# Optimization experiments

Hardware: AMD Instinct MI355X
Metric: run time of the kernel (lower is better)

The kernel has to match this reference:

```python
import jax, jax.numpy as jnp
import numpy as np

MARGIN = 9.0  # args.transe_margin
B, N, D = 32, 200000, 64


def setup_inputs() -> dict:
    key = jax.random.key(0)
    k1, k2, k3 = jax.random.split(key, 3)
    s_emb = jax.random.normal(k1, (B, D), dtype=jnp.float32)
    rel_emb = jax.random.normal(k2, (B, D), dtype=jnp.float32)
    emb_e = jax.random.normal(k3, (N, D), dtype=jnp.float32)
    return {"s_emb": s_emb, "rel_emb": rel_emb, "emb_e": emb_e}


def reference(s_emb, rel_emb, emb_e):
    # mode='rhs': pred = margin - || (s + r)[b,None,:] - emb_e[None,:,:] ||_2 over D
    # dropout with p=0.0 is identity.
    query = s_emb + rel_emb                      # (B, D)
    diff = query[:, None, :] - emb_e[None, :, :]  # (B, N, D) broadcast intermediate
    # stable L2 norm over last dim
    pred = MARGIN - jnp.sqrt(jnp.sum(diff * diff, axis=-1))  # (B, N)
    return pred
```

## Files before the change

kernel.cpp:

```cpp
#include <hip/hip_runtime.h>


#define MARGIN 9.0f

typedef __attribute__((ext_vector_type(8)))  short bf16x8;
typedef __attribute__((ext_vector_type(16))) float f32x16;
typedef __attribute__((ext_vector_type(4)))  unsigned int u32x4;

typedef __attribute__((address_space(3))) void        lds_vp;
typedef __attribute__((address_space(1))) const void  glb_vp;

__device__ __forceinline__ unsigned eswz(unsigned p) {
    return p ^ (((p >> 8) & 15u) << 4);
}

__global__ __launch_bounds__(128, 3)
void transe12(const float* __restrict__ s_emb,
              const float* __restrict__ rel_emb,
              const float* __restrict__ emb_e,
              float* __restrict__ out, int N)
{
    __shared__ __align__(16) char lds[32768];
    const int t = threadIdx.x, w = t >> 6, lane = t & 63;
    const int m = lane & 31, h = lane >> 5;
    char* const b0 = lds + w * 16384;
    char* const b1 = b0 + 8192;
    const int  nt32 = N >> 5;
    const long T0   = (long)blockIdx.x * 8 + w * 4;

    const float4* s4 = (const float4*)s_emb;
    const float4* r4 = (const float4*)rel_emb;
    float4 sv[8], rv[8];
#pragma unroll
    for (int k = 0; k < 8; ++k) sv[k] = s4[k*64 + lane];
#pragma unroll
    for (int k = 0; k < 8; ++k) rv[k] = r4[k*64 + lane];

    auto dma8 = [&](long tile, char* l) {
        const long ts = (tile < nt32) ? tile : (long)(nt32 - 1);
        const char* g = (const char*)emb_e + ts * 8192;
#pragma unroll
        for (int k = 0; k < 8; ++k) {
            const unsigned p = (unsigned)(k*1024 + lane*16);
            __builtin_amdgcn_global_load_lds((glb_vp*)(g + eswz(p)),
                                             (lds_vp*)(l + k*1024), 16, 0, 0);
        }
    };

    dma8(T0 + 1, b1);

#pragma unroll
    for (int k = 0; k < 8; ++k) {
        const unsigned p = (unsigned)(k*1024 + lane*16);
        float4 q = make_float4(sv[k].x+rv[k].x, sv[k].y+rv[k].y,
                               sv[k].z+rv[k].z, sv[k].w+rv[k].w);
        *(float4*)(b0 + eswz(p)) = q;
    }
    asm volatile("s_waitcnt lgkmcnt(0)" ::: "memory");

    const unsigned fb = (unsigned)(m*256 + h*32);
    bf16x8 qh[4], ql[4];
    float qn_part = 0.f;
#pragma unroll
    for (int tt = 0; tt < 4; ++tt) {
        const unsigned pe = eswz(fb + tt*64);
        float4 q0 = *(const float4*)(b0 + pe);
        float4 q1 = *(const float4*)(b0 + (pe ^ 16));
        const float qf[8] = {q0.x,q0.y,q0.z,q0.w, q1.x,q1.y,q1.z,q1.w};
#pragma unroll
        for (int i = 0; i < 8; ++i) {
            const float f = qf[i];
            qn_part = fmaf(f, f, qn_part);
            const unsigned u = __float_as_uint(f);
            qh[tt][i] = (short)(u >> 16);
            const float lo = f - __uint_as_float(u & 0xFFFF0000u);
            ql[tt][i] = (short)(__float_as_uint(lo) >> 16);
        }
    }
    const float qn_own = qn_part + __shfl_xor(qn_part, 32);
    float qn_all[32];
#pragma unroll
    for (int i = 0; i < 32; ++i)
        qn_all[i] = __uint_as_float(
            __builtin_amdgcn_readlane(__float_as_uint(qn_own), i));

    asm volatile("s_waitcnt lgkmcnt(0)" ::: "memory");
    dma8(T0 + 0, b0);

    auto compute_tile = [&](const char* L, f32x16& acc) {
#pragma unroll
        for (int i = 0; i < 16; ++i) acc[i] = 0.f;
        float en_part = 0.f;
#pragma unroll
        for (int tt = 0; tt < 4; ++tt) {
            const unsigned pe = eswz(fb + tt*64);
            float4 e0 = *(const float4*)(L + pe);
            float4 e1 = *(const float4*)(L + (pe ^ 16));
            en_part = fmaf(e0.x, e0.x, en_part);
            en_part = fmaf(e0.y, e0.y, en_part);
            en_part = fmaf(e0.z, e0.z, en_part);
            en_part = fmaf(e0.w, e0.w, en_part);
            en_part = fmaf(e1.x, e1.x, en_part);
            en_part = fmaf(e1.y, e1.y, en_part);
            en_part = fmaf(e1.z, e1.z, en_part);
            en_part = fmaf(e1.w, e1.w, en_part);
            u32x4 ep;
            ep[0] = __builtin_amdgcn_perm(__float_as_uint(e0.y),
                                          __float_as_uint(e0.x), 0x07060302u);
            ep[1] = __builtin_amdgcn_perm(__float_as_uint(e0.w),
                                          __float_as_uint(e0.z), 0x07060302u);
            ep[2] = __builtin_amdgcn_perm(__float_as_uint(e1.y),
                                          __float_as_uint(e1.x), 0x07060302u);
            ep[3] = __builtin_amdgcn_perm(__float_as_uint(e1.w),
                                          __float_as_uint(e1.z), 0x07060302u);
            const bf16x8 eh = __builtin_bit_cast(bf16x8, ep);
            acc = __builtin_amdgcn_mfma_f32_32x32x16_bf16(qh[tt], eh, acc, 0,0,0);
            acc = __builtin_amdgcn_mfma_f32_32x32x16_bf16(ql[tt], eh, acc, 0,0,0);
        }
        const float en = en_part + __shfl_xor(en_part, 32);
#pragma unroll
        for (int r = 0; r < 16; ++r) {
            const int bb = (r & 3) + 8*(r >> 2);
            const float qn_v = h ? qn_all[bb + 4] : qn_all[bb];
            const float d2 = fmaxf(fmaf(-2.f, acc[r], qn_v + en), 0.f);
            acc[r] = MARGIN - sqrtf(d2);
        }
    };

    f32x16 p0, p1, p2, p3;
    asm volatile("s_waitcnt vmcnt(8)" ::: "memory");
    compute_tile(b1, p1);
    asm volatile("s_waitcnt lgkmcnt(0)" ::: "memory");
    dma8(T0 + 2, b1);
    asm volatile("s_waitcnt vmcnt(8)" ::: "memory");
    compute_tile(b0, p0);
    asm volatile("s_waitcnt lgkmcnt(0)" ::: "memory");
    dma8(T0 + 3, b0);
    asm volatile("s_waitcnt vmcnt(8)" ::: "memory");
    compute_tile(b1, p2);
    asm volatile("s_waitcnt vmcnt(0)" ::: "memory");
    compute_tile(b0, p3);

    __syncthreads();
    float* oT = (float*)lds;
    const int nlb = w*128 + m;
#pragma unroll
    for (int r = 0; r < 16; ++r) {
        const int b = (r & 3) + 8*(r >> 2) + 4*h;
        oT[b*256 + nlb +  0] = p0[r];
        oT[b*256 + nlb + 32] = p1[r];
        oT[b*256 + nlb + 64] = p2[r];
        oT[b*256 + nlb + 96] = p3[r];
    }
    __syncthreads();

    const long nb = (long)blockIdx.x * 256;
#pragma unroll
    for (int k = 0; k < 16; ++k) {
        const int  rb  = w*16 + k;
        const long col = nb + lane*4;
        if (col + 3 < N) {
            const float4 v = *(const float4*)(oT + rb*256 + lane*4);
            *(float4*)(out + (size_t)rb * N + col) = v;
        }
    }
}

extern "C" void kernel_launch(void* const* d_in, const int* in_sizes, int n_in,
                              void* d_out, int out_size, void* d_ws, size_t ws_size,
                              hipStream_t stream) {
    const float* s = (const float*)d_in[0];
    const float* r = (const float*)d_in[1];
    const float* e = (const float*)d_in[2];
    float* out = (float*)d_out;

    const int N = in_sizes[2] / 64;
    const int grid = (N + 255) / 256;

    transe12<<<grid, 128, 0, stream>>>(s, r, e, out, N);
}
```

Measured before the change: 20.23 us.

## Switch to 16x16x32 MFMA with 4 waves per 256-column block

Replaces the 32x32x16 bf16 MFMA tiling with 16x16x32 MFMAs computing two 16-row halves of the batch per wave. Blocks grow from 2 to 4 waves, each streaming four 16-entity tiles through smaller double buffers. Query norms are gathered with shuffles instead of 32 readlanes, which cuts register pressure. The goal is more waves in flight to hide memory latency, at the cost of more MFMA instructions and more LDS traffic per entity.

```diff
diff --git a/kernel.cpp b/kernel.cpp
--- a/kernel.cpp
+++ b/kernel.cpp
@@ -3,9 +3,8 @@
 
 #define MARGIN 9.0f
 
-typedef __attribute__((ext_vector_type(8)))  short bf16x8;
-typedef __attribute__((ext_vector_type(16))) float f32x16;
-typedef __attribute__((ext_vector_type(4)))  unsigned int u32x4;
+typedef __attribute__((ext_vector_type(8))) short bf16x8;
+typedef __attribute__((ext_vector_type(4))) float f32x4;
 
 typedef __attribute__((address_space(3))) void        lds_vp;
 typedef __attribute__((address_space(1))) const void  glb_vp;
@@ -14,19 +13,20 @@
     return p ^ (((p >> 8) & 15u) << 4);
 }
 
-__global__ __launch_bounds__(128, 3)
-void transe12(const float* __restrict__ s_emb,
+__global__ __launch_bounds__(256, 4)
+void transe13(const float* __restrict__ s_emb,
               const float* __restrict__ rel_emb,
               const float* __restrict__ emb_e,
               float* __restrict__ out, int N)
 {
     __shared__ __align__(16) char lds[32768];
     const int t = threadIdx.x, w = t >> 6, lane = t & 63;
-    const int m = lane & 31, h = lane >> 5;
-    char* const b0 = lds + w * 16384;
-    char* const b1 = b0 + 8192;
-    const int  nt32 = N >> 5;
-    const long T0   = (long)blockIdx.x * 8 + w * 4;
+    const int c16 = lane & 15;
+    const int g   = lane >> 4;
+    char* const B0 = lds + w * 8192;
+    char* const B1 = B0 + 4096;
+    const int  ntile = N >> 4;
+    const long Tw = (long)blockIdx.x * 16 + w * 4;
 
     const float4* s4 = (const float4*)s_emb;
     const float4* r4 = (const float4*)rel_emb;
@@ -36,128 +36,136 @@
 #pragma unroll
     for (int k = 0; k < 8; ++k) rv[k] = r4[k*64 + lane];
 
-    auto dma8 = [&](long tile, char* l) {
-        const long ts = (tile < nt32) ? tile : (long)(nt32 - 1);
-        const char* g = (const char*)emb_e + ts * 8192;
+    auto dma4 = [&](long tile, char* l) {
+        const long ts = (tile < ntile) ? tile : (long)(ntile - 1);
+        const char* gp = (const char*)emb_e + ts * 4096;
 #pragma unroll
-        for (int k = 0; k < 8; ++k) {
+        for (int k = 0; k < 4; ++k) {
             const unsigned p = (unsigned)(k*1024 + lane*16);
-            __builtin_amdgcn_global_load_lds((glb_vp*)(g + eswz(p)),
+            __builtin_amdgcn_global_load_lds((glb_vp*)(gp + eswz(p)),
                                              (lds_vp*)(l + k*1024), 16, 0, 0);
         }
     };
+    dma4(Tw + 0, B1);
 
-    dma8(T0 + 1, b1);
+    const unsigned fbase = (unsigned)(c16*256 + g*32);
+    bf16x8 qh[2][2], ql[2][2];
+    float qnp[2];
+#pragma unroll
+    for (int mh = 0; mh < 2; ++mh) {
+#pragma unroll
+        for (int k = 0; k < 4; ++k) {
+            const int kk = mh*4 + k;
+            const unsigned p = (unsigned)(k*1024 + lane*16);
+            float4 q = make_float4(sv[kk].x+rv[kk].x, sv[kk].y+rv[kk].y,
+                                   sv[kk].z+rv[kk].z, sv[kk].w+rv[kk].w);
+            *(float4*)(B0 + eswz(p)) = q;
+        }
+        asm volatile("s_waitcnt lgkmcnt(0)" ::: "memory");
+        float qq = 0.f;
+#pragma unroll
+        for (int ks = 0; ks < 2; ++ks) {
+            const unsigned pe = eswz(fbase + ks*128);
+            float4 q0 = *(const float4*)(B0 + pe);
+            float4 q1 = *(const float4*)(B0 + (pe ^ 16));
+            const float qf[8] = {q0.x,q0.y,q0.z,q0.w, q1.x,q1.y,q1.z,q1.w};
+#pragma unroll
+            for (int i = 0; i < 8; ++i) {
+                const float f = qf[i];
+                qq = fmaf(f, f, qq);
+                const unsigned u = __float_as_uint(f);
+                qh[mh][ks][i] = (short)(u >> 16);
+                const float lo = f - __uint_as_float(u & 0xFFFF0000u);
+                ql[mh][ks][i] = (short)(__float_as_uint(lo) >> 16);
+            }
+        }
+        qnp[mh] = qq;
+        asm volatile("s_waitcnt lgkmcnt(0)" ::: "memory");
+    }
+    dma4(Tw + 1, B0);
 
+    float qn0 = qnp[0]; qn0 += __shfl_xor(qn0, 16); qn0 += __shfl_xor(qn0, 32);
+    float qn1 = qnp[1]; qn1 += __shfl_xor(qn1, 16); qn1 += __shfl_xor(qn1, 32);
+    float qn_need[8];
 #pragma unroll
-    for (int k = 0; k < 8; ++k) {
-        const unsigned p = (unsigned)(k*1024 + lane*16);
-        float4 q = make_float4(sv[k].x+rv[k].x, sv[k].y+rv[k].y,
-                               sv[k].z+rv[k].z, sv[k].w+rv[k].w);
-        *(float4*)(b0 + eswz(p)) = q;
+    for (int j = 0; j < 4; ++j) {
+        qn_need[j]     = __shfl(qn0, g*4 + j);
+        qn_need[4 + j] = __shfl(qn1, g*4 + j);
     }
-    asm volatile("s_waitcnt lgkmcnt(0)" ::: "memory");
 
-    const unsigned fb = (unsigned)(m*256 + h*32);
-    bf16x8 qh[4], ql[4];
-    float qn_part = 0.f;
+    auto tile_full = [&](const char* L, f32x4& o0, f32x4& o1) {
+        f32x4 a0 = {0.f,0.f,0.f,0.f}, a1 = {0.f,0.f,0.f,0.f};
+        float ep = 0.f;
 #pragma unroll
-    for (int tt = 0; tt < 4; ++tt) {
-        const unsigned pe = eswz(fb + tt*64);
-        float4 q0 = *(const float4*)(b0 + pe);
-        float4 q1 = *(const float4*)(b0 + (pe ^ 16));
-        const float qf[8] = {q0.x,q0.y,q0.z,q0.w, q1.x,q1.y,q1.z,q1.w};
-#pragma unroll
-        for (int i = 0; i < 8; ++i) {
-            const float f = qf[i];
-            qn_part = fmaf(f, f, qn_part);
-            const unsigned u = __float_as_uint(f);
-            qh[tt][i] = (short)(u >> 16);
-            const float lo = f - __uint_as_float(u & 0xFFFF0000u);
-            ql[tt][i] = (short)(__float_as_uint(lo) >> 16);
-        }
-    }
-    const float qn_own = qn_part + __shfl_xor(qn_part, 32);
-    float qn_all[32];
-#pragma unroll
-    for (int i = 0; i < 32; ++i)
-        qn_all[i] = __uint_as_float(
-            __builtin_amdgcn_readlane(__float_as_uint(qn_own), i));
-
-    asm volatile("s_waitcnt lgkmcnt(0)" ::: "memory");
-    dma8(T0 + 0, b0);
-
-    auto compute_tile = [&](const char* L, f32x16& acc) {
-#pragma unroll
-        for (int i = 0; i < 16; ++i) acc[i] = 0.f;
-        float en_part = 0.f;
-#pragma unroll
-        for (int tt = 0; tt < 4; ++tt) {
-            const unsigned pe = eswz(fb + tt*64);
+        for (int ks = 0; ks < 2; ++ks) {
+            const unsigned pe = eswz(fbase + ks*128);
             float4 e0 = *(const float4*)(L + pe);
             float4 e1 = *(const float4*)(L + (pe ^ 16));
-            en_part = fmaf(e0.x, e0.x, en_part);
-            en_part = fmaf(e0.y, e0.y, en_part);
-            en_part = fmaf(e0.z, e0.z, en_part);
-            en_part = fmaf(e0.w, e0.w, en_part);
-            en_part = fmaf(e1.x, e1.x, en_part);
-            en_part = fmaf(e1.y, e1.y, en_part);
-            en_part = fmaf(e1.z, e1.z, en_part);
-            en_part = fmaf(e1.w, e1.w, en_part);
-            u32x4 ep;
-            ep[0] = __builtin_amdgcn_perm(__float_as_uint(e0.y),
+            ep = fmaf(e0.x, e0.x, ep); ep = fmaf(e0.y, e0.y, ep);
+            ep = fmaf(e0.z, e0.z, ep); ep = fmaf(e0.w, e0.w, ep);
+            ep = fmaf(e1.x, e1.x, ep); ep = fmaf(e1.y, e1.y, ep);
+            ep = fmaf(e1.z, e1.z, ep); ep = fmaf(e1.w, e1.w, ep);
+            unsigned ew[4];
+            ew[0] = __builtin_amdgcn_perm(__float_as_uint(e0.y),
                                           __float_as_uint(e0.x), 0x07060302u);
-            ep[1] = __builtin_amdgcn_perm(__float_as_uint(e0.w),
+            ew[1] = __builtin_amdgcn_perm(__float_as_uint(e0.w),
                                           __float_as_uint(e0.z), 0x07060302u);
-            ep[2] = __builtin_amdgcn_perm(__float_as_uint(e1.y),
+            ew[2] = __builtin_amdgcn_perm(__float_as_uint(e1.y),
                                           __float_as_uint(e1.x), 0x07060302u);
-            ep[3] = __builtin_amdgcn_perm(__float_as_uint(e1.w),
+            ew[3] = __builtin_amdgcn_perm(__float_as_uint(e1.w),
                                           __float_as_uint(e1.z), 0x07060302u);
-            const bf16x8 eh = __builtin_bit_cast(bf16x8, ep);
-            acc = __builtin_amdgcn_mfma_f32_32x32x16_bf16(qh[tt], eh, acc, 0,0,0);
-            acc = __builtin_amdgcn_mfma_f32_32x32x16_bf16(ql[tt], eh, acc, 0,0,0);
+            bf16x8 eh;
+            __builtin_memcpy(&eh, ew, 16);
+            a0 = __builtin_amdgcn_mfma_f32_16x16x32_bf16(qh[0][ks], eh, a0, 0,0,0);
+            a0 = __builtin_amdgcn_mfma_f32_16x16x32_bf16(ql[0][ks], eh, a0, 0,0,0);
+            a1 = __builtin_amdgcn_mfma_f32_16x16x32_bf16(qh[1][ks], eh, a1, 0,0,0);
+            a1 = __builtin_amdgcn_mfma_f32_16x16x32_bf16(ql[1][ks], eh, a1, 0,0,0);
         }
-        const float en = en_part + __shfl_xor(en_part, 32);
+        float en = ep; en += __shfl_xor(en, 16); en += __shfl_xor(en, 32);
 #pragma unroll
-        for (int r = 0; r < 16; ++r) {
-            const int bb = (r & 3) + 8*(r >> 2);
-            const float qn_v = h ? qn_all[bb + 4] : qn_all[bb];
-            const float d2 = fmaxf(fmaf(-2.f, acc[r], qn_v + en), 0.f);
-            acc[r] = MARGIN - sqrtf(d2);
+        for (int j = 0; j < 4; ++j) {
+            const float d0 = fmaxf(fmaf(-2.f, a0[j], qn_need[j]     + en), 0.f);
+            const float d1 = fmaxf(fmaf(-2.f, a1[j], qn_need[4 + j] + en), 0.f);
+            o0[j] = MARGIN - sqrtf(d0);
+            o1[j] = MARGIN - sqrtf(d1);
         }
     };
 
-    f32x16 p0, p1, p2, p3;
-    asm volatile("s_waitcnt vmcnt(8)" ::: "memory");
-    compute_tile(b1, p1);
+    f32x4 p00, p01, p10, p11, p20, p21, p30, p31;
+    asm volatile("s_waitcnt vmcnt(4)" ::: "memory");
+    tile_full(B1, p00, p01);
     asm volatile("s_waitcnt lgkmcnt(0)" ::: "memory");
-    dma8(T0 + 2, b1);
-    asm volatile("s_waitcnt vmcnt(8)" ::: "memory");
-    compute_tile(b0, p0);
+    dma4(Tw + 2, B1);
+    asm volatile("s_waitcnt vmcnt(4)" ::: "memory");
+    tile_full(B0, p10, p11);
     asm volatile("s_waitcnt lgkmcnt(0)" ::: "memory");
-    dma8(T0 + 3, b0);
-    asm volatile("s_waitcnt vmcnt(8)" ::: "memory");
-    compute_tile(b1, p2);
+    dma4(Tw + 3, B0);
+    asm volatile("s_waitcnt vmcnt(4)" ::: "memory");
+    tile_full(B1, p20, p21);
     asm volatile("s_waitcnt vmcnt(0)" ::: "memory");
-    compute_tile(b0, p3);
+    tile_full(B0, p30, p31);
 
     __syncthreads();
     float* oT = (float*)lds;
-    const int nlb = w*128 + m;
+    const int nl = w*64 + c16;
 #pragma unroll
-    for (int r = 0; r < 16; ++r) {
-        const int b = (r & 3) + 8*(r >> 2) + 4*h;
-        oT[b*256 + nlb +  0] = p0[r];
-        oT[b*256 + nlb + 32] = p1[r];
-        oT[b*256 + nlb + 64] = p2[r];
-        oT[b*256 + nlb + 96] = p3[r];
+    for (int j = 0; j < 4; ++j) {
+        const int b0r = g*4 + j, b1r = 16 + g*4 + j;
+        oT[b0r*256 + nl +  0] = p00[j];
+        oT[b1r*256 + nl +  0] = p01[j];
+        oT[b0r*256 + nl + 16] = p10[j];
+        oT[b1r*256 + nl + 16] = p11[j];
+        oT[b0r*256 + nl + 32] = p20[j];
+        oT[b1r*256 + nl + 32] = p21[j];
+        oT[b0r*256 + nl + 48] = p30[j];
+        oT[b1r*256 + nl + 48] = p31[j];
     }
     __syncthreads();
 
     const long nb = (long)blockIdx.x * 256;
 #pragma unroll
-    for (int k = 0; k < 16; ++k) {
-        const int  rb  = w*16 + k;
+    for (int k = 0; k < 8; ++k) {
+        const int  rb  = w*8 + k;
         const long col = nb + lane*4;
         if (col + 3 < N) {
             const float4 v = *(const float4*)(oT + rb*256 + lane*4);
@@ -177,5 +185,5 @@
     const int N = in_sizes[2] / 64;
     const int grid = (N + 255) / 256;
 
-    transe12<<<grid, 128, 0, stream>>>(s, r, e, out, N);
+    transe13<<<grid, 256, 0, stream>>>(s, r, e, out, N);
 }
```

After: 20.66 us. 2.1% more time.

## Load entity tiles into registers and stage to LDS instead of direct DMA

Applied to the files above, without the earlier changes.

Replaces the direct global-to-LDS DMA of emb_e tiles with register loads through inline asm, written into LDS just before each tile is computed. s_emb and rel_emb now go straight to LDS by DMA, and their sum is formed when the query fragments are read. Occupancy hint drops from 3 to 2 waves per EU, and scheduling barriers are added. The goal is to issue all tile loads up front with simpler waits, at the cost of more registers and extra LDS write traffic per tile.

```diff
diff --git a/kernel.cpp b/kernel.cpp
--- a/kernel.cpp
+++ b/kernel.cpp
@@ -14,8 +14,12 @@
     return p ^ (((p >> 8) & 15u) << 4);
 }
 
-__global__ __launch_bounds__(128, 3)
-void transe12(const float* __restrict__ s_emb,
+#define VMWAIT(n) do { \
+    asm volatile("s_waitcnt vmcnt(" #n ")" ::: "memory"); \
+    __builtin_amdgcn_sched_barrier(0); } while (0)
+
+__global__ __launch_bounds__(128, 2)
+void transe17(const float* __restrict__ s_emb,
               const float* __restrict__ rel_emb,
               const float* __restrict__ emb_e,
               float* __restrict__ out, int N)
@@ -28,17 +32,7 @@
     const int  nt32 = N >> 5;
     const long T0   = (long)blockIdx.x * 8 + w * 4;
 
-    const float4* s4 = (const float4*)s_emb;
-    const float4* r4 = (const float4*)rel_emb;
-    float4 sv[8], rv[8];
-#pragma unroll
-    for (int k = 0; k < 8; ++k) sv[k] = s4[k*64 + lane];
-#pragma unroll
-    for (int k = 0; k < 8; ++k) rv[k] = r4[k*64 + lane];
-
-    auto dma8 = [&](long tile, char* l) {
-        const long ts = (tile < nt32) ? tile : (long)(nt32 - 1);
-        const char* g = (const char*)emb_e + ts * 8192;
+    auto dma8g = [&](const char* g, char* l) {
 #pragma unroll
         for (int k = 0; k < 8; ++k) {
             const unsigned p = (unsigned)(k*1024 + lane*16);
@@ -46,27 +40,36 @@
                                              (lds_vp*)(l + k*1024), 16, 0, 0);
         }
     };
+    dma8g((const char*)s_emb,   b0);
+    dma8g((const char*)rel_emb, b1);
+    __builtin_amdgcn_sched_barrier(0);
 
-    dma8(T0 + 1, b1);
+    float4 E0[8], E1[8];
+    auto eload = [&](long tile, float4 (&E)[8]) {
+        const long ts = (tile < nt32) ? tile : (long)(nt32 - 1);
+        const char* g = (const char*)emb_e + ts * 8192 + (unsigned)(lane * 16);
+#pragma unroll
+        for (int k = 0; k < 8; ++k) {
+            asm volatile("global_load_dwordx4 %0, %1, off"
+                         : "=&v"(E[k]) : "v"(g + k*1024) : "memory");
+        }
+    };
+    eload(T0 + 0, E0);
+    eload(T0 + 1, E1);
 
-#pragma unroll
-    for (int k = 0; k < 8; ++k) {
-        const unsigned p = (unsigned)(k*1024 + lane*16);
-        float4 q = make_float4(sv[k].x+rv[k].x, sv[k].y+rv[k].y,
-                               sv[k].z+rv[k].z, sv[k].w+rv[k].w);
-        *(float4*)(b0 + eswz(p)) = q;
-    }
-    asm volatile("s_waitcnt lgkmcnt(0)" ::: "memory");
-
+    VMWAIT(16);
     const unsigned fb = (unsigned)(m*256 + h*32);
     bf16x8 qh[4], ql[4];
     float qn_part = 0.f;
 #pragma unroll
     for (int tt = 0; tt < 4; ++tt) {
         const unsigned pe = eswz(fb + tt*64);
-        float4 q0 = *(const float4*)(b0 + pe);
-        float4 q1 = *(const float4*)(b0 + (pe ^ 16));
-        const float qf[8] = {q0.x,q0.y,q0.z,q0.w, q1.x,q1.y,q1.z,q1.w};
+        float4 s0 = *(const float4*)(b0 + pe);
+        float4 s1 = *(const float4*)(b0 + (pe ^ 16));
+        float4 r0 = *(const float4*)(b1 + pe);
+        float4 r1 = *(const float4*)(b1 + (pe ^ 16));
+        const float qf[8] = { s0.x+r0.x, s0.y+r0.y, s0.z+r0.z, s0.w+r0.w,
+                              s1.x+r1.x, s1.y+r1.y, s1.z+r1.z, s1.w+r1.w };
 #pragma unroll
         for (int i = 0; i < 8; ++i) {
             const float f = qf[i];
@@ -83,9 +86,16 @@
     for (int i = 0; i < 32; ++i)
         qn_all[i] = __uint_as_float(
             __builtin_amdgcn_readlane(__float_as_uint(qn_own), i));
+    asm volatile("s_waitcnt lgkmcnt(0)" ::: "memory");
+    __builtin_amdgcn_sched_barrier(0);
 
-    asm volatile("s_waitcnt lgkmcnt(0)" ::: "memory");
-    dma8(T0 + 0, b0);
+    auto stage = [&](const float4 (&E)[8], char* l) {
+#pragma unroll
+        for (int k = 0; k < 8; ++k) {
+            const unsigned p = (unsigned)(k*1024 + lane*16);
+            *(float4*)(l + eswz(p)) = E[k];
+        }
+    };
 
     auto compute_tile = [&](const char* L, f32x16& acc) {
 #pragma unroll
@@ -128,18 +138,20 @@
     };
 
     f32x16 p0, p1, p2, p3;
-    asm volatile("s_waitcnt vmcnt(8)" ::: "memory");
+    VMWAIT(8);
+    stage(E0, b0);
+    eload(T0 + 2, E0);
+    compute_tile(b0, p0);
+    VMWAIT(8);
+    stage(E1, b1);
+    eload(T0 + 3, E1);
     compute_tile(b1, p1);
-    asm volatile("s_waitcnt lgkmcnt(0)" ::: "memory");
-    dma8(T0 + 2, b1);
-    asm volatile("s_waitcnt vmcnt(8)" ::: "memory");
-    compute_tile(b0, p0);
-    asm volatile("s_waitcnt lgkmcnt(0)" ::: "memory");
-    dma8(T0 + 3, b0);
-    asm volatile("s_waitcnt vmcnt(8)" ::: "memory");
-    compute_tile(b1, p2);
-    asm volatile("s_waitcnt vmcnt(0)" ::: "memory");
-    compute_tile(b0, p3);
+    VMWAIT(8);
+    stage(E0, b0);
+    compute_tile(b0, p2);
+    VMWAIT(0);
+    stage(E1, b1);
+    compute_tile(b1, p3);
 
     __syncthreads();
     float* oT = (float*)lds;
@@ -177,5 +189,5 @@
     const int N = in_sizes[2] / 64;
     const int grid = (N + 255) / 256;
 
-    transe12<<<grid, 128, 0, stream>>>(s, r, e, out, N);
+    transe17<<<grid, 128, 0, stream>>>(s, r, e, out, N);
 }
```

After: 22.24 us. 1.1x slower.
